# Kernel optimization log

Hardware: AMD Instinct MI355X
Metric: run time of the kernel (lower is better)

Reference implementation:

```python
import jax, jax.numpy as jnp
import numpy as np

EMB, HEADS, LAT, FFN = 1024, 16, 256, 4096
HD = EMB // HEADS
B, N = 2, 2048

def _ln(x, w, b, eps=1e-5):
    mu = jnp.mean(x, axis=-1, keepdims=True)
    var = jnp.var(x, axis=-1, keepdims=True)
    return (x - mu) * jax.lax.rsqrt(var + eps) * w + b

def setup_inputs() -> dict:
    key = jax.random.key(0)
    ks = jax.random.split(key, 16)
    def lin(k, fan_in, fan_out):
        bound = 1.0 / np.sqrt(fan_in)
        kw, kb = jax.random.split(k)
        W = jax.random.uniform(kw, (fan_in, fan_out), jnp.float32, -bound, bound)
        b = jax.random.uniform(kb, (fan_out,), jnp.float32, -bound, bound)
        return W, b
    Wq, bq = lin(ks[0], EMB, EMB)
    WaK, baK = lin(ks[1], EMB, LAT)
    WbK, bbK = lin(ks[2], LAT, EMB)
    WaV, baV = lin(ks[3], EMB, LAT)
    WbV, bbV = lin(ks[4], LAT, EMB)
    Wo, bo = lin(ks[5], EMB, EMB)
    W1, b1 = lin(ks[6], EMB, FFN)
    W2, b2 = lin(ks[7], FFN, EMB)
    return {
        'x': jax.random.normal(ks[8], (B, N, EMB), jnp.float32),
        'attn_bias': jax.random.normal(ks[9], (N, N), jnp.float32),
        'Wq': Wq, 'bq': bq, 'WaK': WaK, 'baK': baK, 'WbK': WbK, 'bbK': bbK,
        'WaV': WaV, 'baV': baV, 'WbV': WbV, 'bbV': bbV, 'Wo': Wo, 'bo': bo,
        'W1': W1, 'b1': b1, 'W2': W2, 'b2': b2,
        'ln1_w': jnp.ones((EMB,), jnp.float32), 'ln1_b': jnp.zeros((EMB,), jnp.float32),
        'ln2_w': jnp.ones((EMB,), jnp.float32), 'ln2_b': jnp.zeros((EMB,), jnp.float32),
    }

def reference(x, attn_bias, Wq, bq, WaK, baK, WbK, bbK, WaV, baV, WbV, bbV,
              Wo, bo, W1, b1, W2, b2, ln1_w, ln1_b, ln2_w, ln2_b):
    Q = x @ Wq + bq                       # [B,N,E]
    K = (x @ WaK + baK) @ WbK + bbK       # low-rank K
    V = (x @ WaV + baV) @ WbV + bbV       # low-rank V
    def split(t):
        return t.reshape(B, N, HEADS, HD).transpose(0, 2, 1, 3)  # [B,H,N,D]
    Qh, Kh, Vh = split(Q), split(K), split(V)
    scores = jnp.einsum('bhnd,bhmd->bhnm', Qh, Kh) / np.sqrt(HD)
    scores = scores + attn_bias[None, None]
    weights = jax.nn.softmax(scores, axis=-1)
    attn = jnp.einsum('bhnm,bhmd->bhnd', weights, Vh)
    attn = attn.transpose(0, 2, 1, 3).reshape(B, N, EMB)
    attn = attn @ Wo + bo
    h = _ln(x + attn, ln1_w, ln1_b)
    ffn = jax.nn.gelu(h @ W1 + b1, approximate=False) @ W2 + b2
    return _ln(h + ffn, ln2_w, ln2_b)
```

## Files before the change

### kernel.cpp

```cpp
#include <hip/hip_runtime.h>
#include <hip/hip_bf16.h>
#include <math.h>

typedef unsigned short u16;
typedef short bf16x8 __attribute__((ext_vector_type(8)));
typedef float f32x4 __attribute__((ext_vector_type(4)));

#define EMB   1024
#define HEADS 16
#define HD    64
#define LATD  256
#define FFND  4096
#define BATCH 2
#define SEQ   2048
#define TOK   (BATCH*SEQ)

#define SCL2  0.18033688011112042f
#define LOG2E 1.4426950408889634f

__device__ __forceinline__ float bf2f(u16 u) {
    union { unsigned int i; float f; } x; x.i = ((unsigned int)u) << 16; return x.f;
}
__device__ __forceinline__ u16 f2bf(float f) {
    union { float f; unsigned int i; } x; x.f = f;
    unsigned int i = x.i;
    unsigned int lsb = (i >> 16) & 1u;
    i += 0x7fffu + lsb;
    return (u16)(i >> 16);
}
__device__ __forceinline__ void gld16(const u16* g, u16* l) {
    __builtin_amdgcn_global_load_lds(
        (const __attribute__((address_space(1))) void*)g,
        (__attribute__((address_space(3))) void*)l, 16, 0, 0);
}
__device__ __forceinline__ unsigned int cvt_pk_bf16(float a, float b) {
    unsigned int r;
    asm("v_cvt_pk_bf16_f32 %0, %1, %2" : "=v"(r) : "v"(a), "v"(b));
    return r;
}
#if defined(__has_builtin)
#if __has_builtin(__builtin_amdgcn_exp2f)
#define EXP2(x) __builtin_amdgcn_exp2f(x)
#endif
#endif
#ifndef EXP2
#define EXP2(x) exp2f(x)
#endif

__global__ __launch_bounds__(256) void cvt_f32_bf16_kernel(
    const float* __restrict__ in, u16* __restrict__ out, int n8)
{
    int i = blockIdx.x * 256 + threadIdx.x;
    int stride = gridDim.x * 256;
    for (; i < n8; i += stride) {
        float4 f0 = *(const float4*)(in + (size_t)i * 8);
        float4 f1 = *(const float4*)(in + (size_t)i * 8 + 4);
        u16 e[8];
        e[0] = f2bf(f0.x); e[1] = f2bf(f0.y); e[2] = f2bf(f0.z); e[3] = f2bf(f0.w);
        e[4] = f2bf(f1.x); e[5] = f2bf(f1.y); e[6] = f2bf(f1.z); e[7] = f2bf(f1.w);
        *(uint4*)(out + (size_t)i * 8) = *(const uint4*)e;
    }
}

__global__ __launch_bounds__(256) void prep_bias_kernel(
    const float* __restrict__ a, const float* __restrict__ b,
    const float* __restrict__ q, float* __restrict__ bKV, float* __restrict__ bqs)
{
    int i = blockIdx.x * 256 + threadIdx.x;
    if (i < 256)      bKV[i] = a[i];
    else if (i < 512) bKV[i] = b[i - 256];
    else              bqs[i - 512] = q[i - 512] * SCL2;
}

__global__ __launch_bounds__(256) void permute_ab_kernel(
    const float* __restrict__ ab, float* __restrict__ abP)
{
    const int kt = blockIdx.x, qt = blockIdx.y;
    const int tid = threadIdx.x;
    const int lane = tid & 63, wq = tid >> 6;
    const int qq = lane >> 4, col = lane & 15;
#pragma unroll
    for (int wi = wq; wi < 8; wi += 4)
#pragma unroll
        for (int mt = 0; mt < 4; mt++) {
            float4 v = *(const float4*)(ab + (size_t)(qt * 128 + wi * 16 + col) * SEQ
                                        + kt * 64 + mt * 16 + qq * 4);
            v.x *= LOG2E; v.y *= LOG2E; v.z *= LOG2E; v.w *= LOG2E;
            *(float4*)(abP + (((size_t)qt * 32 + kt) * 8 + wi) * 1024 + mt * 256 + lane * 4) = v;
        }
}

struct TDesc { const float* src; u16* dst; int K; int N; int ofs; float scl; };
struct TTable { TDesc d[8]; };

__global__ __launch_bounds__(256) void transpose_all_kernel(TTable tt)
{
    __shared__ u16 t[32][33];
    int tb = blockIdx.x, e = 0;
#pragma unroll
    for (int i = 1; i < 8; i++) if (tb >= tt.d[i].ofs) e = i;
    const float* src = tt.d[e].src;
    u16* dst = tt.d[e].dst;
    const int K = tt.d[e].K, N = tt.d[e].N;
    const float scl = tt.d[e].scl;
    const int local = tb - tt.d[e].ofs;
    const int nx = N >> 5;
    const int bx = (local % nx) * 32;
    const int by = (local / nx) * 32;
    const int tx = threadIdx.x & 31;
    const int ty = threadIdx.x >> 5;
#pragma unroll
    for (int i = 0; i < 32; i += 8)
        t[ty + i][tx] = f2bf(src[(size_t)(by + ty + i) * N + bx + tx] * scl);
    __syncthreads();
#pragma unroll
    for (int i = 0; i < 32; i += 8)
        dst[(size_t)(bx + ty + i) * K + by + tx] = t[tx][ty + i];
}

__device__ __forceinline__ void xcd_swz(int& bx, int& by)
{
    const int gx = gridDim.x;
    const int nwg = gx * gridDim.y;
    const int flat = blockIdx.x + gx * blockIdx.y;
    const int swz = (flat & 7) * (nwg >> 3) + (flat >> 3);
    bx = swz % gx;
    by = swz / gx;
}

#define BM 128
#define GBK 64

template <int ACT, int BNv, int TRC>
__device__ __forceinline__ void gemm_body(
    const u16* __restrict__ A, int lda, const u16* __restrict__ WT,
    const float* __restrict__ bias, u16* __restrict__ C,
    int K, int N, int bx, int by, u16* Al, u16* Wl, u16* Tl)
{
    const int NT = BNv / 32;
    const int WN = BNv / 2;
    const int CW = BNv / 32;

    const int tid  = threadIdx.x;
    const int lane = tid & 63;
    const int w    = tid >> 6;
    const int wm = w >> 1, wn = w & 1;
    const int col = lane & 15, qq = lane >> 4;
    const size_t bm = (size_t)by * BM;
    const size_t bn = (size_t)bx * BNv;

    f32x4 acc[4][NT];
#pragma unroll
    for (int mt = 0; mt < 4; mt++)
#pragma unroll
        for (int nt = 0; nt < NT; nt++) acc[mt][nt] = (f32x4){0.f, 0.f, 0.f, 0.f};

    const u16* gA[4]; u16* lA[4];
#pragma unroll
    for (int i = 0; i < 4; i++) {
        int f = w * 256 + i * 64 + lane;
        int r = f >> 3, s = f & 7, sg = s ^ (r & 7);
        gA[i] = A + (bm + r) * (size_t)lda + sg * 8;
        lA[i] = &Al[(size_t)(w * 256 + i * 64) * 8];
    }
    const u16* gW[4]; u16* lW[4];
#pragma unroll
    for (int i = 0; i < CW; i++) {
        int f = w * (BNv * 2) + i * 64 + lane;
        int r = f >> 3, s = f & 7, sg = s ^ (r & 7);
        gW[i] = WT + (bn + r) * (size_t)K + sg * 8;
        lW[i] = &Wl[(size_t)(w * (BNv * 2) + i * 64) * 8];
    }

    for (int k0 = 0; k0 < K; k0 += GBK) {
#pragma unroll
        for (int i = 0; i < 4; i++) gld16(gA[i] + k0, lA[i]);
#pragma unroll
        for (int i = 0; i < CW; i++) gld16(gW[i] + k0, lW[i]);
        __syncthreads();

#pragma unroll
        for (int kk = 0; kk < 2; kk++) {
            bf16x8 af[4], bfr[NT];
#pragma unroll
            for (int mt = 0; mt < 4; mt++) {
                int rr = wm * 64 + mt * 16 + col;
                int sub = (kk * 4 + qq) ^ (rr & 7);
                af[mt] = *(const bf16x8*)&Al[rr * GBK + sub * 8];
            }
#pragma unroll
            for (int nt = 0; nt < NT; nt++) {
                int rn = wn * WN + nt * 16 + col;
                int sub = (kk * 4 + qq) ^ (rn & 7);
                bfr[nt] = *(const bf16x8*)&Wl[rn * GBK + sub * 8];
            }
#pragma unroll
            for (int mt = 0; mt < 4; mt++)
#pragma unroll
                for (int nt = 0; nt < NT; nt++)
                    acc[mt][nt] = __builtin_amdgcn_mfma_f32_16x16x32_bf16(
                        af[mt], bfr[nt], acc[mt][nt], 0, 0, 0);
        }
        __syncthreads();
    }

    float bv[NT];
#pragma unroll
    for (int nt = 0; nt < NT; nt++)
        bv[nt] = bias[bn + wn * WN + nt * 16 + col];

    if (TRC) {
#pragma unroll
        for (int mt = 0; mt < 4; mt++)
#pragma unroll
            for (int nt = 0; nt < NT; nt++)
#pragma unroll
                for (int r = 0; r < 4; r++) {
                    float v = acc[mt][nt][r] + bv[nt];
                    Tl[(wn * WN + nt * 16 + col) * 136 + (wm * 64 + mt * 16 + qq * 4 + r)] = f2bf(v);
                }
        __syncthreads();
        const int b_ = (int)(bm >> 11);
        const size_t tokb = bm & (SEQ - 1);
        const int row = tid >> 2;
        u16* dst = C + ((size_t)b_ * EMB + (size_t)bx * 64 + row) * SEQ + tokb;
        const u16* srcl = Tl + row * 136;
#pragma unroll
        for (int j = 0; j < 4; j++) {
            int c0 = ((tid & 3) + j * 4) * 8;
            *(uint4*)(dst + c0) = *(const uint4*)(srcl + c0);
        }
        return;
    }

#pragma unroll
    for (int mt = 0; mt < 4; mt++) {
#pragma unroll
        for (int nt = 0; nt < NT; nt++) {
#pragma unroll
            for (int r = 0; r < 4; r++) {
                float v = acc[mt][nt][r] + bv[nt];
                if (ACT == 1) v = 0.5f * v * (1.0f + erff(v * 0.70710678118654752f));
                size_t rg = bm + wm * 64 + mt * 16 + qq * 4 + r;
                C[rg * (size_t)N + bn + wn * WN + nt * 16 + col] = f2bf(v);
            }
        }
    }
}

template <int ACT, int BNv, int MINW>
__global__ __launch_bounds__(256, MINW) void gemm_bt_kernel(
    const u16* __restrict__ A, int lda, const u16* __restrict__ WT,
    const float* __restrict__ bias, u16* __restrict__ C,
    int K, int N)
{
    __shared__ __align__(16) u16 Al[BM * GBK];
    __shared__ __align__(16) u16 Wl[BNv * GBK];
    int bx, by;
    xcd_swz(bx, by);
    gemm_body<ACT, BNv, 0>(A, lda, WT, bias, C, K, N, bx, by, Al, Wl, Al);
}

struct GPair {
    const u16* A0; const u16* A1;
    const u16* W0; const u16* W1;
    const float* b0; const float* b1;
    u16* C0; u16* C1;
    int lda0, lda1, N0, N1, nx0;
};

template <int BNv, int MINW, int TRV>
__global__ __launch_bounds__(256, MINW) void gemm_pair_kernel(GPair p, int K)
{
    __shared__ __align__(16) u16 SH[BM * GBK + BNv * GBK];
    u16* Al = SH;
    u16* Wl = SH + BM * GBK;
    int bxs, by;
    xcd_swz(bxs, by);
    const bool s1 = bxs >= p.nx0;
    const u16* A = s1 ? p.A1 : p.A0;
    const u16* WT = s1 ? p.W1 : p.W0;
    const float* bias = s1 ? p.b1 : p.b0;
    u16* C = s1 ? p.C1 : p.C0;
    const int lda = s1 ? p.lda1 : p.lda0;
    const int N = s1 ? p.N1 : p.N0;
    const int bx = s1 ? bxs - p.nx0 : bxs;
    if (TRV && s1)
        gemm_body<0, BNv, 1>(A, lda, WT, bias, C, K, N, bx, by, Al, Wl, SH);
    else
        gemm_body<0, BNv, 0>(A, lda, WT, bias, C, K, N, bx, by, Al, Wl, SH);
}

#define BQ   128
#define BKV  64
#define NKVT (SEQ / BKV)
#define LDK  72
#define LDP  72
#define LDV  72

__global__ __launch_bounds__(512, 4) void fattn_kernel(
    const u16* __restrict__ Q, const u16* __restrict__ K,
    const u16* __restrict__ VT, const float* __restrict__ abP,
    u16* __restrict__ O)
{
    __shared__ __align__(16) u16 Ks[2][BKV * LDK];
    __shared__ __align__(16) u16 Vt[2][HD * LDV];
    __shared__ __align__(16) u16 Ps[BQ * LDP];

    const int tid = threadIdx.x;
    const int lane = tid & 63;
    const int w = tid >> 6;
    const int col = lane & 15, qq = lane >> 4;
    const int qt = blockIdx.x;
    const int b = blockIdx.y >> 4, h = blockIdx.y & 15;
    const size_t tok0 = (size_t)b * SEQ + (size_t)qt * BQ;
    const int wrow = w * 16;
    const size_t kvbase = (size_t)b * SEQ * EMB + h * HD;
    const size_t vtb = ((size_t)b * EMB + h * HD) * SEQ;

    const int krow = tid >> 3, kcol = (tid & 7) * 8;

    bf16x8 aq[2];
#pragma unroll
    for (int kk = 0; kk < 2; kk++)
        aq[kk] = *(const bf16x8*)(Q + (tok0 + wrow + col) * EMB + h * HD + kk * 32 + qq * 8);

    float m_st = -1e30f, l_st = 0.f;
    f32x4 o_acc[4];
#pragma unroll
    for (int dt = 0; dt < 4; dt++) o_acc[dt] = (f32x4){0.f, 0.f, 0.f, 0.f};

    uint4 kreg, vreg;
#define LOADKV(KV0) do {                                                              \
        kreg = *(const uint4*)(K + kvbase + (size_t)((KV0) + krow) * EMB + kcol);     \
        vreg = *(const uint4*)(VT + vtb + (size_t)krow * SEQ + (KV0) + kcol);         \
    } while (0)

    LOADKV(0);
    *(uint4*)&Ks[0][krow * LDK + kcol] = kreg;
    *(uint4*)&Vt[0][krow * LDV + kcol] = vreg;
    __syncthreads();
    LOADKV(BKV);

    const float* abq = abP + (size_t)qt * NKVT * 8192 + (size_t)w * 1024;
    f32x4 abv[4];
#pragma unroll
    for (int mt = 0; mt < 4; mt++)
        abv[mt] = *(const f32x4*)(abq + mt * 256 + lane * 4);

    for (int t = 0; t < NKVT; t++) {
        const int cur = t & 1;
        const u16* Kc = Ks[cur];

        f32x4 s2[4];
#pragma unroll
        for (int mt = 0; mt < 4; mt++) s2[mt] = abv[mt];
        __builtin_amdgcn_s_setprio(1);
#pragma unroll
        for (int mt = 0; mt < 4; mt++) {
            bf16x8 ak0 = *(const bf16x8*)&Kc[(mt * 16 + col) * LDK + qq * 8];
            bf16x8 ak1 = *(const bf16x8*)&Kc[(mt * 16 + col) * LDK + 32 + qq * 8];
            s2[mt] = __builtin_amdgcn_mfma_f32_16x16x32_bf16(ak0, aq[0], s2[mt], 0, 0, 0);
            s2[mt] = __builtin_amdgcn_mfma_f32_16x16x32_bf16(ak1, aq[1], s2[mt], 0, 0, 0);
        }
        __builtin_amdgcn_s_setprio(0);

        if (t + 1 < NKVT) {
            const float* abn = abq + (size_t)(t + 1) * 8192;
#pragma unroll
            for (int mt = 0; mt < 4; mt++)
                abv[mt] = *(const f32x4*)(abn + mt * 256 + lane * 4);
        }

        if (t + 1 < NKVT) {
            *(uint4*)&Ks[cur ^ 1][krow * LDK + kcol] = kreg;
            *(uint4*)&Vt[cur ^ 1][krow * LDV + kcol] = vreg;
        }
        if (t + 2 < NKVT) LOADKV((t + 2) * BKV);

        float t0 = fmaxf(fmaxf(s2[0][0], s2[0][1]), fmaxf(s2[0][2], s2[0][3]));
        float t1 = fmaxf(fmaxf(s2[1][0], s2[1][1]), fmaxf(s2[1][2], s2[1][3]));
        float t2 = fmaxf(fmaxf(s2[2][0], s2[2][1]), fmaxf(s2[2][2], s2[2][3]));
        float t3 = fmaxf(fmaxf(s2[3][0], s2[3][1]), fmaxf(s2[3][2], s2[3][3]));
        float tm = fmaxf(fmaxf(t0, t1), fmaxf(t2, t3));
        tm = fmaxf(tm, __shfl_xor(tm, 16));
        tm = fmaxf(tm, __shfl_xor(tm, 32));
        if (!__all(tm <= m_st + 8.f)) {
            float mnew = fmaxf(m_st, tm);
            float alpha = EXP2(m_st - mnew);
            m_st = mnew;
            l_st *= alpha;
#pragma unroll
            for (int dt = 0; dt < 4; dt++)
#pragma unroll
                for (int r = 0; r < 4; r++) o_acc[dt][r] *= alpha;
        }
        float rs = 0.f;
#pragma unroll
        for (int mt = 0; mt < 4; mt++)
#pragma unroll
            for (int r = 0; r < 4; r++) {
                float e = EXP2(s2[mt][r] - m_st);
                s2[mt][r] = e;
                rs += e;
            }
        rs += __shfl_xor(rs, 16);
        rs += __shfl_xor(rs, 32);
        l_st += rs;

#pragma unroll
        for (int mt = 0; mt < 4; mt++) {
            uint2 pp;
            pp.x = cvt_pk_bf16(s2[mt][0], s2[mt][1]);
            pp.y = cvt_pk_bf16(s2[mt][2], s2[mt][3]);
            *(uint2*)&Ps[(wrow + col) * LDP + mt * 16 + qq * 4] = pp;
        }

        __builtin_amdgcn_s_setprio(1);
#pragma unroll
        for (int kk = 0; kk < 2; kk++) {
            bf16x8 ap = *(const bf16x8*)&Ps[(wrow + col) * LDP + kk * 32 + qq * 8];
#pragma unroll
            for (int dt = 0; dt < 4; dt++) {
                bf16x8 bv = *(const bf16x8*)&Vt[cur][(dt * 16 + col) * LDV + kk * 32 + qq * 8];
                o_acc[dt] = __builtin_amdgcn_mfma_f32_16x16x32_bf16(bv, ap, o_acc[dt], 0, 0, 0);
            }
        }
        __builtin_amdgcn_s_setprio(0);
        __syncthreads();
    }
#undef LOADKV

    float lr = 1.0f / l_st;
#pragma unroll
    for (int dt = 0; dt < 4; dt++) {
        uint2 pp;
        pp.x = cvt_pk_bf16(o_acc[dt][0] * lr, o_acc[dt][1] * lr);
        pp.y = cvt_pk_bf16(o_acc[dt][2] * lr, o_acc[dt][3] * lr);
        *(uint2*)(O + (tok0 + wrow + col) * EMB + h * HD + dt * 16 + qq * 4) = pp;
    }
}

template <int AF32, int OUTF32>
__global__ __launch_bounds__(256) void ln_kernel(
    const void* __restrict__ A, const u16* __restrict__ R,
    const float* __restrict__ w, const float* __restrict__ bb,
    void* __restrict__ out)
{
    __shared__ float r1[4], r2[4];
    const int tid = threadIdx.x;
    const size_t row = blockIdx.x;
    const int c0 = tid * 4;

    float v[4];
    {
        float a[4];
        if (AF32) {
            float4 av = *(const float4*)((const float*)A + row * EMB + c0);
            a[0] = av.x; a[1] = av.y; a[2] = av.z; a[3] = av.w;
        } else {
            ushort4 av = *(const ushort4*)((const u16*)A + row * EMB + c0);
            a[0] = bf2f(av.x); a[1] = bf2f(av.y); a[2] = bf2f(av.z); a[3] = bf2f(av.w);
        }
        ushort4 rv = *(const ushort4*)(R + row * EMB + c0);
        v[0] = a[0] + bf2f(rv.x); v[1] = a[1] + bf2f(rv.y);
        v[2] = a[2] + bf2f(rv.z); v[3] = a[3] + bf2f(rv.w);
    }
    float s = (v[0] + v[1]) + (v[2] + v[3]);
    float s2 = (v[0] * v[0] + v[1] * v[1]) + (v[2] * v[2] + v[3] * v[3]);

#pragma unroll
    for (int o = 32; o > 0; o >>= 1) {
        s  += __shfl_down(s, o);
        s2 += __shfl_down(s2, o);
    }
    if ((tid & 63) == 0) { r1[tid >> 6] = s; r2[tid >> 6] = s2; }
    __syncthreads();
    s  = r1[0] + r1[1] + r1[2] + r1[3];
    s2 = r2[0] + r2[1] + r2[2] + r2[3];

    float mu = s * (1.0f / EMB);
    float var = s2 * (1.0f / EMB) - mu * mu;
    float rs = rsqrtf(var + 1e-5f);

    float4 wv = *(const float4*)(w + c0);
    float4 bv = *(const float4*)(bb + c0);
    float y0 = (v[0] - mu) * rs * wv.x + bv.x;
    float y1 = (v[1] - mu) * rs * wv.y + bv.y;
    float y2 = (v[2] - mu) * rs * wv.z + bv.z;
    float y3 = (v[3] - mu) * rs * wv.w + bv.w;
    if (OUTF32) {
        *(float4*)((float*)out + row * EMB + c0) = make_float4(y0, y1, y2, y3);
    } else {
        ushort4 ov;
        ov.x = f2bf(y0); ov.y = f2bf(y1); ov.z = f2bf(y2); ov.w = f2bf(y3);
        *(ushort4*)((u16*)out + row * EMB + c0) = ov;
    }
}

extern "C" void kernel_launch(void* const* d_in, const int* in_sizes, int n_in,
                              void* d_out, int out_size, void* d_ws, size_t ws_size,
                              hipStream_t stream)
{
    const float* x    = (const float*)d_in[0];
    const float* ab   = (const float*)d_in[1];
    const float* Wq   = (const float*)d_in[2];
    const float* bq   = (const float*)d_in[3];
    const float* WaK  = (const float*)d_in[4];
    const float* baK  = (const float*)d_in[5];
    const float* WbK  = (const float*)d_in[6];
    const float* bbK  = (const float*)d_in[7];
    const float* WaV  = (const float*)d_in[8];
    const float* baV  = (const float*)d_in[9];
    const float* WbV  = (const float*)d_in[10];
    const float* bbV  = (const float*)d_in[11];
    const float* Wo   = (const float*)d_in[12];
    const float* bo   = (const float*)d_in[13];
    const float* W1   = (const float*)d_in[14];
    const float* b1   = (const float*)d_in[15];
    const float* W2   = (const float*)d_in[16];
    const float* b2   = (const float*)d_in[17];
    const float* ln1w = (const float*)d_in[18];
    const float* ln1b = (const float*)d_in[19];
    const float* ln2w = (const float*)d_in[20];
    const float* ln2b = (const float*)d_in[21];

    u16* w = (u16*)d_ws;
    size_t o = 0;
    u16* WqT  = w + o; o += (size_t)EMB * EMB;
    u16* WaKT = w + o; o += (size_t)EMB * LATD;
    u16* WaVT = w + o; o += (size_t)EMB * LATD;
    u16* WbKT = w + o; o += (size_t)LATD * EMB;
    u16* WbVT = w + o; o += (size_t)LATD * EMB;
    u16* WoT  = w + o; o += (size_t)EMB * EMB;
    u16* W1T  = w + o; o += (size_t)EMB * FFND;
    u16* W2T  = w + o; o += (size_t)FFND * EMB;
    u16* Qb   = w + o; o += (size_t)TOK * EMB;
    u16* Kb   = w + o; o += (size_t)TOK * EMB;
    u16* Vb   = w + o; o += (size_t)TOK * EMB;
    u16* aOb  = w + o; o += (size_t)TOK * EMB;
    u16* projb= w + o; o += (size_t)TOK * EMB;
    u16* hb   = w + o; o += (size_t)TOK * EMB;
    u16* xb   = w + o; o += (size_t)TOK * EMB;
    float* bKV = (float*)(w + o); o += 1024;
    float* bqs = (float*)(w + o); o += 2048;
    float* abP = (float*)projb;
    u16* KVa = aOb;
    u16* f1  = Qb;
    u16* f2  = projb;

    dim3 blk(256);

    cvt_f32_bf16_kernel<<<dim3(2048), blk, 0, stream>>>(x, xb, TOK * EMB / 8);
    prep_bias_kernel<<<dim3(6), blk, 0, stream>>>(baK, baV, bq, bKV, bqs);
    permute_ab_kernel<<<dim3(32, 16), blk, 0, stream>>>(ab, abP);

    TTable tt;
    tt.d[0] = {Wq,  WqT,  EMB,  EMB,  0,    SCL2};
    tt.d[1] = {WaK, WaKT, EMB,  LATD, 1024, 1.0f};
    tt.d[2] = {WaV, WaVT, EMB,  LATD, 1280, 1.0f};
    tt.d[3] = {WbK, WbKT, LATD, EMB,  1536, 1.0f};
    tt.d[4] = {WbV, WbVT, LATD, EMB,  1792, 1.0f};
    tt.d[5] = {Wo,  WoT,  EMB,  EMB,  2048, 1.0f};
    tt.d[6] = {W1,  W1T,  EMB,  FFND, 3072, 1.0f};
    tt.d[7] = {W2,  W2T,  FFND, EMB,  7168, 1.0f};
    transpose_all_kernel<<<dim3(11264), blk, 0, stream>>>(tt);

    {
        GPair p;
        p.A0 = xb;  p.A1 = xb;
        p.W0 = WqT; p.W1 = WaKT;
        p.b0 = bqs; p.b1 = bKV;
        p.C0 = Qb;  p.C1 = KVa;
        p.lda0 = EMB; p.lda1 = EMB;
        p.N0 = EMB; p.N1 = 512; p.nx0 = 16;
        gemm_pair_kernel<64, 3, 0><<<dim3(24, TOK / BM), blk, 0, stream>>>(p, EMB);
    }
    {
        GPair p;
        p.A0 = KVa;  p.A1 = KVa + LATD;
        p.W0 = WbKT; p.W1 = WbVT;
        p.b0 = bbK;  p.b1 = bbV;
        p.C0 = Kb;   p.C1 = Vb;
        p.lda0 = 512; p.lda1 = 512;
        p.N0 = EMB; p.N1 = EMB; p.nx0 = 16;
        gemm_pair_kernel<64, 3, 1><<<dim3(32, TOK / BM), blk, 0, stream>>>(p, LATD);
    }

    fattn_kernel<<<dim3(SEQ / BQ, BATCH * HEADS), dim3(512), 0, stream>>>(Qb, Kb, Vb, abP, aOb);

    gemm_bt_kernel<0,64,3><<<dim3(EMB / 64, TOK / BM), blk, 0, stream>>>(aOb, EMB, WoT, bo, projb, EMB, EMB);

    ln_kernel<1,0><<<dim3(TOK), blk, 0, stream>>>(x, projb, ln1w, ln1b, hb);

    gemm_bt_kernel<1,128,2><<<dim3(FFND / 128, TOK / BM), blk, 0, stream>>>(hb, EMB, W1T, b1, f1, EMB, FFND);
    gemm_bt_kernel<0,64,3><<<dim3(EMB / 64, TOK / BM), blk, 0, stream>>>(f1, FFND, W2T, b2, f2, FFND, EMB);

    ln_kernel<0,1><<<dim3(TOK), blk, 0, stream>>>(hb, f2, ln2w, ln2b, (float*)d_out);
}
```

Before: 380.0 us.

## Merge prep kernels into one launch and store attention bias as bf16

Folds the input conversion, bias prep, attention-bias permute and weight transposes into a single kernel launch, removing three launch boundaries. The permuted attention bias (pre-scaled by log2e) is now stored as bf16 instead of fp32, halving the bias bytes that every flash-attention block streams per KV tile. The bias is unpacked back to fp32 in registers before the MFMA accumulate. Bias precision drops to bf16, which may add small error in the softmax logits.

Result: no change. 379.9 us (-0.0%).

```diff
diff --git a/kernel.cpp b/kernel.cpp
--- a/kernel.cpp
+++ b/kernel.cpp
@@ -21,6 +21,12 @@
 __device__ __forceinline__ float bf2f(u16 u) {
     union { unsigned int i; float f; } x; x.i = ((unsigned int)u) << 16; return x.f;
 }
+__device__ __forceinline__ float bfLO(unsigned int u) {
+    union { unsigned int i; float f; } x; x.i = u << 16; return x.f;
+}
+__device__ __forceinline__ float bfHI(unsigned int u) {
+    union { unsigned int i; float f; } x; x.i = u & 0xffff0000u; return x.f;
+}
 __device__ __forceinline__ u16 f2bf(float f) {
     union { float f; unsigned int i; } x; x.f = f;
     unsigned int i = x.i;
@@ -47,75 +53,81 @@
 #define EXP2(x) exp2f(x)
 #endif
 
-__global__ __launch_bounds__(256) void cvt_f32_bf16_kernel(
-    const float* __restrict__ in, u16* __restrict__ out, int n8)
-{
-    int i = blockIdx.x * 256 + threadIdx.x;
-    int stride = gridDim.x * 256;
-    for (; i < n8; i += stride) {
-        float4 f0 = *(const float4*)(in + (size_t)i * 8);
-        float4 f1 = *(const float4*)(in + (size_t)i * 8 + 4);
+struct TDesc { const float* src; u16* dst; int K; int N; int ofs; float scl; };
+struct TTable { TDesc d[8]; };
+
+struct PrepArgs {
+    const float* x; u16* xb;
+    const float* baK; const float* baV; const float* bq; float* bKV; float* bqs;
+    const float* ab; u16* abP;
+    TTable tt;
+};
+
+__global__ __launch_bounds__(256) void prep_all_kernel(PrepArgs pa)
+{
+    __shared__ u16 t[32][33];
+    int blk = blockIdx.x;
+    const int tid = threadIdx.x;
+
+    if (blk < 2048) {
+        int i = blk * 256 + tid;
+        float4 f0 = *(const float4*)(pa.x + (size_t)i * 8);
+        float4 f1 = *(const float4*)(pa.x + (size_t)i * 8 + 4);
         u16 e[8];
         e[0] = f2bf(f0.x); e[1] = f2bf(f0.y); e[2] = f2bf(f0.z); e[3] = f2bf(f0.w);
         e[4] = f2bf(f1.x); e[5] = f2bf(f1.y); e[6] = f2bf(f1.z); e[7] = f2bf(f1.w);
-        *(uint4*)(out + (size_t)i * 8) = *(const uint4*)e;
-    }
-}
-
-__global__ __launch_bounds__(256) void prep_bias_kernel(
-    const float* __restrict__ a, const float* __restrict__ b,
-    const float* __restrict__ q, float* __restrict__ bKV, float* __restrict__ bqs)
-{
-    int i = blockIdx.x * 256 + threadIdx.x;
-    if (i < 256)      bKV[i] = a[i];
-    else if (i < 512) bKV[i] = b[i - 256];
-    else              bqs[i - 512] = q[i - 512] * SCL2;
-}
-
-__global__ __launch_bounds__(256) void permute_ab_kernel(
-    const float* __restrict__ ab, float* __restrict__ abP)
-{
-    const int kt = blockIdx.x, qt = blockIdx.y;
-    const int tid = threadIdx.x;
-    const int lane = tid & 63, wq = tid >> 6;
-    const int qq = lane >> 4, col = lane & 15;
-#pragma unroll
-    for (int wi = wq; wi < 8; wi += 4)
-#pragma unroll
-        for (int mt = 0; mt < 4; mt++) {
-            float4 v = *(const float4*)(ab + (size_t)(qt * 128 + wi * 16 + col) * SEQ
-                                        + kt * 64 + mt * 16 + qq * 4);
-            v.x *= LOG2E; v.y *= LOG2E; v.z *= LOG2E; v.w *= LOG2E;
-            *(float4*)(abP + (((size_t)qt * 32 + kt) * 8 + wi) * 1024 + mt * 256 + lane * 4) = v;
-        }
-}
-
-struct TDesc { const float* src; u16* dst; int K; int N; int ofs; float scl; };
-struct TTable { TDesc d[8]; };
-
-__global__ __launch_bounds__(256) void transpose_all_kernel(TTable tt)
-{
-    __shared__ u16 t[32][33];
-    int tb = blockIdx.x, e = 0;
-#pragma unroll
-    for (int i = 1; i < 8; i++) if (tb >= tt.d[i].ofs) e = i;
-    const float* src = tt.d[e].src;
-    u16* dst = tt.d[e].dst;
-    const int K = tt.d[e].K, N = tt.d[e].N;
-    const float scl = tt.d[e].scl;
-    const int local = tb - tt.d[e].ofs;
-    const int nx = N >> 5;
-    const int bx = (local % nx) * 32;
-    const int by = (local / nx) * 32;
-    const int tx = threadIdx.x & 31;
-    const int ty = threadIdx.x >> 5;
-#pragma unroll
-    for (int i = 0; i < 32; i += 8)
-        t[ty + i][tx] = f2bf(src[(size_t)(by + ty + i) * N + bx + tx] * scl);
-    __syncthreads();
-#pragma unroll
-    for (int i = 0; i < 32; i += 8)
-        dst[(size_t)(bx + ty + i) * K + by + tx] = t[tx][ty + i];
+        *(uint4*)(pa.xb + (size_t)i * 8) = *(const uint4*)e;
+        return;
+    }
+    blk -= 2048;
+    if (blk < 6) {
+        int i = blk * 256 + tid;
+        if (i < 256)      pa.bKV[i] = pa.baK[i];
+        else if (i < 512) pa.bKV[i] = pa.baV[i - 256];
+        else              pa.bqs[i - 512] = pa.bq[i - 512] * SCL2;
+        return;
+    }
+    blk -= 6;
+    if (blk < 512) {
+        const int kt = blk & 31, qt = blk >> 5;
+        const int lane = tid & 63, wq = tid >> 6;
+        const int qq = lane >> 4, col = lane & 15;
+#pragma unroll
+        for (int wi = wq; wi < 8; wi += 4)
+#pragma unroll
+            for (int mt = 0; mt < 4; mt++) {
+                float4 v = *(const float4*)(pa.ab + (size_t)(qt * 128 + wi * 16 + col) * SEQ
+                                            + kt * 64 + mt * 16 + qq * 4);
+                uint2 pk;
+                pk.x = cvt_pk_bf16(v.x * LOG2E, v.y * LOG2E);
+                pk.y = cvt_pk_bf16(v.z * LOG2E, v.w * LOG2E);
+                *(uint2*)(pa.abP + (((size_t)qt * 32 + kt) * 8 + wi) * 1024 + mt * 256 + lane * 4) = pk;
+            }
+        return;
+    }
+    blk -= 512;
+    {
+        int tb = blk, e = 0;
+#pragma unroll
+        for (int i = 1; i < 8; i++) if (tb >= pa.tt.d[i].ofs) e = i;
+        const float* src = pa.tt.d[e].src;
+        u16* dst = pa.tt.d[e].dst;
+        const int K = pa.tt.d[e].K, N = pa.tt.d[e].N;
+        const float scl = pa.tt.d[e].scl;
+        const int local = tb - pa.tt.d[e].ofs;
+        const int nx = N >> 5;
+        const int bx = (local % nx) * 32;
+        const int by = (local / nx) * 32;
+        const int tx = tid & 31;
+        const int ty = tid >> 5;
+#pragma unroll
+        for (int i = 0; i < 32; i += 8)
+            t[ty + i][tx] = f2bf(src[(size_t)(by + ty + i) * N + bx + tx] * scl);
+        __syncthreads();
+#pragma unroll
+        for (int i = 0; i < 32; i += 8)
+            dst[(size_t)(bx + ty + i) * K + by + tx] = t[tx][ty + i];
+    }
 }
 
 __device__ __forceinline__ void xcd_swz(int& bx, int& by)
@@ -300,7 +312,7 @@
 
 __global__ __launch_bounds__(512, 4) void fattn_kernel(
     const u16* __restrict__ Q, const u16* __restrict__ K,
-    const u16* __restrict__ VT, const float* __restrict__ abP,
+    const u16* __restrict__ VT, const u16* __restrict__ abP,
     u16* __restrict__ O)
 {
     __shared__ __align__(16) u16 Ks[2][BKV * LDK];
@@ -342,11 +354,11 @@
     __syncthreads();
     LOADKV(BKV);
 
-    const float* abq = abP + (size_t)qt * NKVT * 8192 + (size_t)w * 1024;
-    f32x4 abv[4];
+    const u16* abq = abP + (size_t)qt * NKVT * 8192 + (size_t)w * 1024;
+    uint2 abr[4];
 #pragma unroll
     for (int mt = 0; mt < 4; mt++)
-        abv[mt] = *(const f32x4*)(abq + mt * 256 + lane * 4);
+        abr[mt] = *(const uint2*)(abq + mt * 256 + lane * 4);
 
     for (int t = 0; t < NKVT; t++) {
         const int cur = t & 1;
@@ -354,7 +366,12 @@
 
         f32x4 s2[4];
 #pragma unroll
-        for (int mt = 0; mt < 4; mt++) s2[mt] = abv[mt];
+        for (int mt = 0; mt < 4; mt++) {
+            s2[mt][0] = bfLO(abr[mt].x);
+            s2[mt][1] = bfHI(abr[mt].x);
+            s2[mt][2] = bfLO(abr[mt].y);
+            s2[mt][3] = bfHI(abr[mt].y);
+        }
         __builtin_amdgcn_s_setprio(1);
 #pragma unroll
         for (int mt = 0; mt < 4; mt++) {
@@ -366,10 +383,10 @@
         __builtin_amdgcn_s_setprio(0);
 
         if (t + 1 < NKVT) {
-            const float* abn = abq + (size_t)(t + 1) * 8192;
+            const u16* abn = abq + (size_t)(t + 1) * 8192;
 #pragma unroll
             for (int mt = 0; mt < 4; mt++)
-                abv[mt] = *(const f32x4*)(abn + mt * 256 + lane * 4);
+                abr[mt] = *(const uint2*)(abn + mt * 256 + lane * 4);
         }
 
         if (t + 1 < NKVT) {
@@ -544,27 +561,26 @@
     u16* xb   = w + o; o += (size_t)TOK * EMB;
     float* bKV = (float*)(w + o); o += 1024;
     float* bqs = (float*)(w + o); o += 2048;
-    float* abP = (float*)projb;
+    u16* abP = projb;
     u16* KVa = aOb;
     u16* f1  = Qb;
     u16* f2  = projb;
 
     dim3 blk(256);
 
-    cvt_f32_bf16_kernel<<<dim3(2048), blk, 0, stream>>>(x, xb, TOK * EMB / 8);
-    prep_bias_kernel<<<dim3(6), blk, 0, stream>>>(baK, baV, bq, bKV, bqs);
-    permute_ab_kernel<<<dim3(32, 16), blk, 0, stream>>>(ab, abP);
-
-    TTable tt;
-    tt.d[0] = {Wq,  WqT,  EMB,  EMB,  0,    SCL2};
-    tt.d[1] = {WaK, WaKT, EMB,  LATD, 1024, 1.0f};
-    tt.d[2] = {WaV, WaVT, EMB,  LATD, 1280, 1.0f};
-    tt.d[3] = {WbK, WbKT, LATD, EMB,  1536, 1.0f};
-    tt.d[4] = {WbV, WbVT, LATD, EMB,  1792, 1.0f};
-    tt.d[5] = {Wo,  WoT,  EMB,  EMB,  2048, 1.0f};
-    tt.d[6] = {W1,  W1T,  EMB,  FFND, 3072, 1.0f};
-    tt.d[7] = {W2,  W2T,  FFND, EMB,  7168, 1.0f};
-    transpose_all_kernel<<<dim3(11264), blk, 0, stream>>>(tt);
+    PrepArgs pa;
+    pa.x = x; pa.xb = xb;
+    pa.baK = baK; pa.baV = baV; pa.bq = bq; pa.bKV = bKV; pa.bqs = bqs;
+    pa.ab = ab; pa.abP = abP;
+    pa.tt.d[0] = {Wq,  WqT,  EMB,  EMB,  0,    SCL2};
+    pa.tt.d[1] = {WaK, WaKT, EMB,  LATD, 1024, 1.0f};
+    pa.tt.d[2] = {WaV, WaVT, EMB,  LATD, 1280, 1.0f};
+    pa.tt.d[3] = {WbK, WbKT, LATD, EMB,  1536, 1.0f};
+    pa.tt.d[4] = {WbV, WbVT, LATD, EMB,  1792, 1.0f};
+    pa.tt.d[5] = {Wo,  WoT,  EMB,  EMB,  2048, 1.0f};
+    pa.tt.d[6] = {W1,  W1T,  EMB,  FFND, 3072, 1.0f};
+    pa.tt.d[7] = {W2,  W2T,  FFND, EMB,  7168, 1.0f};
+    prep_all_kernel<<<dim3(13830), blk, 0, stream>>>(pa);
 
     {
         GPair p;
```
